# Kernel tuning notes

Measured on AMD Instinct MI355X. Metric: run time of the kernel, lower is better.

Reference implementation:

```python
import jax, jax.numpy as jnp
import numpy as np


def setup_inputs() -> dict:
    key = jax.random.key(0)
    ks = jax.random.split(key, 8)
    B, N, F, H, D, C = 16, 8192, 512, 512, 256, 2
    s = 0.02
    return {
        "h": jax.random.normal(ks[0], (B, N, F), dtype=jnp.float32),
        "W1": jax.random.normal(ks[1], (F, H), dtype=jnp.float32) * s,
        "b1": jnp.zeros((H,), jnp.float32),
        "Wa": jax.random.normal(ks[2], (H, D), dtype=jnp.float32) * s,
        "ba": jnp.zeros((D,), jnp.float32),
        "Wb": jax.random.normal(ks[3], (H, D), dtype=jnp.float32) * s,
        "bb": jnp.zeros((D,), jnp.float32),
        "Wc": jax.random.normal(ks[4], (D, 1), dtype=jnp.float32) * s,
        "bc": jnp.zeros((1,), jnp.float32),
        "Wcls": jax.random.normal(ks[5], (H, C), dtype=jnp.float32) * s,
        "bcls": jnp.zeros((C,), jnp.float32),
    }


def reference(h, W1, b1, Wa, ba, Wb, bb, Wc, bc, Wcls, bcls):
    # h: [B, N, F]  (B bags, N instances each)
    h1 = jax.nn.relu(jnp.einsum("bnf,fh->bnh", h, W1) + b1)        # [B,N,H]
    a = jnp.tanh(jnp.einsum("bnh,hd->bnd", h1, Wa) + ba)           # [B,N,D]
    g = jax.nn.sigmoid(jnp.einsum("bnh,hd->bnd", h1, Wb) + bb)     # [B,N,D]
    A = jnp.einsum("bnd,dk->bnk", a * g, Wc) + bc                  # [B,N,1]
    A_raw = jnp.swapaxes(A, 1, 2)                                  # [B,1,N]
    A_sm = jax.nn.softmax(A_raw, axis=-1)                          # [B,1,N]
    M = jnp.einsum("bkn,bnh->bkh", A_sm, h1)                       # [B,1,H]
    context = jnp.mean(M, axis=0)                                  # [1,H]  (sum / len(h_list))
    logits = context @ Wcls + bcls                                 # [1,C]
    Y_prob = jax.nn.softmax(logits, axis=1)
    Y_hat = jnp.argmax(logits, axis=1, keepdims=True)
    return (logits, Y_prob, Y_hat, A_raw, M)
```

## Files before the change

### kernel.cpp

```cpp
#include <hip/hip_runtime.h>
#include <math.h>

typedef short bf16x8 __attribute__((ext_vector_type(8)));
typedef float f32x4  __attribute__((ext_vector_type(4)));

#define GLOAD_LDS16(SRC, DST) \
  __builtin_amdgcn_global_load_lds((const __attribute__((address_space(1))) void*)(SRC), \
      (__attribute__((address_space(3))) void*)(DST), 16, 0, 0)

#define WAITVM(N) asm volatile("s_waitcnt vmcnt(" #N ")" ::: "memory")
#define WAITLGKM0 asm volatile("s_waitcnt lgkmcnt(0)" ::: "memory")
#define BARRIER() do { __builtin_amdgcn_s_barrier(); asm volatile("" ::: "memory"); } while (0)

__device__ __forceinline__ unsigned short f2bf(float f) {
  union { float f; unsigned u; } v; v.f = f;
  unsigned r = v.u + 0x7FFFu + ((v.u >> 16) & 1u);
  return (unsigned short)(r >> 16);
}
__device__ __forceinline__ float bf2f(unsigned short s) {
  union { unsigned u; float f; } v; v.u = ((unsigned)s) << 16;
  return v.f;
}
__device__ __forceinline__ unsigned pk2bf(float lo, float hi) {
  unsigned r;
  asm("v_cvt_pk_bf16_f32 %0, %1, %2" : "=v"(r) : "v"(lo), "v"(hi));
  return r;
}
__device__ __forceinline__ float fexp2(float x) {
  float r; asm("v_exp_f32 %0, %1" : "=v"(r) : "v"(x)); return r;
}
__device__ __forceinline__ float frcp(float x) {
  float r; asm("v_rcp_f32 %0, %1" : "=v"(r) : "v"(x)); return r;
}
#define LOG2E 1.44269504f
__device__ __forceinline__ float fexp(float x) { return fexp2(x * LOG2E); }


__global__ void carp_wpack(const float* __restrict__ W1, const float* __restrict__ Wa,
                           const float* __restrict__ Wb,
                           unsigned short* __restrict__ W1T_pk, unsigned short* __restrict__ WabT_pk) {
  int t = blockIdx.x * 256 + threadIdx.x;
  int mat = t >> 15;
  int gid = t & 32767;
  int g = gid & 511;
  int kt = (gid >> 9) & 15;
  int p = gid >> 13;
  int s = g >> 6, l = g & 63;
  int j = p * 128 + s * 16 + (l & 15);
  int k = kt * 32 + (l >> 4) * 8;
  unsigned short v[8];
  if (mat == 0) {
#pragma unroll
    for (int e = 0; e < 8; ++e) v[e] = f2bf(W1[(size_t)(k + e) * 512 + j]);
    *(uint4*)(W1T_pk + (size_t)gid * 8) = *(const uint4*)v;
  } else {
    int d = j >> 1;
    const float* Wx = (j & 1) ? Wb : Wa;
#pragma unroll
    for (int e = 0; e < 8; ++e) v[e] = f2bf(Wx[(size_t)(k + e) * 256 + d]);
    *(uint4*)(WabT_pk + (size_t)gid * 8) = *(const uint4*)v;
  }
}

__launch_bounds__(512, 2)
__global__ void carp_gemm1(const float* __restrict__ h, const unsigned short* __restrict__ W1T_pk,
                           const float* __restrict__ b1, unsigned short* __restrict__ h1_pk) {
  __shared__ __align__(16) unsigned short lds[49152];
  int bid0 = blockIdx.x;
  int bid = (bid0 & 7) * 256 + (bid0 >> 3);
  int bn = bid & 3, bm = bid >> 2;
  int brow = bm * 256;
  int tid = threadIdx.x, lane = tid & 63, wid = tid >> 6;
  int wr = wid >> 1, wc = wid & 1;

  f32x4 acc[4][4] = {};
  float4 ar[8];

  int r0 = tid >> 4;
  int chunk = tid & 15;
  const float* hbase = h + (size_t)(brow + r0) * 512 + chunk * 4;
  int kgA = (chunk & 7) >> 1, r16A = r0 & 15;
  int aw_const = (chunk >> 3) * 8192 + (r0 >> 4) * 1024 + kgA * 256
               + ((r16A * 16) ^ (kgA << 5)) + (chunk & 1) * 8;
  int aread_lane = (lane >> 4) * 256 + (((lane & 15) * 16) ^ ((lane >> 4) << 5));

#define G1_LOADA(TP) do { \
  _Pragma("unroll") for (int q = 0; q < 8; ++q) \
    ar[q] = *(const float4*)(hbase + (size_t)(q * 32) * 512 + (TP) * 64); \
  } while (0)
#define G1_WRITEA(TP) do { \
  char* dstA = (char*)lds + ((TP) & 1) * 32768; \
  _Pragma("unroll") for (int q = 0; q < 8; ++q) { \
    uint2 wv; wv.x = pk2bf(ar[q].x, ar[q].y); wv.y = pk2bf(ar[q].z, ar[q].w); \
    *(uint2*)(dstA + (q >> 2) * 16384 + (q & 3) * 2048 + aw_const) = wv; \
  } } while (0)
#define G1_STAGEB(TP, BUF) do { \
  _Pragma("unroll") for (int t2 = 0; t2 < 2; ++t2) \
    GLOAD_LDS16(W1T_pk + ((size_t)(bn * 16 + (TP) * 2 + t2) * 512 + wid * 64 + lane) * 8, \
                (char*)lds + 65536 + (BUF) * 16384 + t2 * 8192 + (size_t)wid * 1024); \
  } while (0)

  G1_LOADA(0);
  WAITVM(0);
  G1_WRITEA(0);
  G1_STAGEB(0, 0);
  G1_LOADA(1);
  WAITLGKM0;

#pragma unroll 1
  for (int tp = 0; tp < 8; ++tp) {
    if (tp < 7) G1_STAGEB(tp + 1, (tp + 1) & 1);
    if (tp < 7) { WAITVM(10); } else { WAITVM(0); }
    BARRIER();
    const char* Abase = (const char*)lds + (tp & 1) * 32768;
    const char* Bbase = (const char*)lds + 65536 + (tp & 1) * 16384;
#pragma unroll
    for (int tt = 0; tt < 2; ++tt) {
      bf16x8 afr[4], bfr[4];
#pragma unroll
      for (int m = 0; m < 4; ++m) {
        int gs = wr * 4 + m;
        afr[m] = *(const bf16x8*)(Abase + (gs >> 3) * 16384 + tt * 8192
                                  + (gs & 7) * 1024 + aread_lane);
      }
#pragma unroll
      for (int n = 0; n < 4; ++n)
        bfr[n] = *(const bf16x8*)(Bbase + tt * 8192 + (size_t)((wc * 4 + n) * 64 + lane) * 16);
#pragma unroll
      for (int m = 0; m < 4; ++m)
#pragma unroll
        for (int n = 0; n < 4; ++n)
          acc[m][n] = __builtin_amdgcn_mfma_f32_16x16x32_bf16(afr[m], bfr[n], acc[m][n], 0, 0, 0);
    }
    if (tp < 7) { WAITVM(2); G1_WRITEA(tp + 1); }
    if (tp < 6) G1_LOADA(tp + 2);
    WAITLGKM0;
    BARRIER();
  }
#undef G1_LOADA
#undef G1_WRITEA
#undef G1_STAGEB

  unsigned short* img = lds;
#pragma unroll
  for (int n = 0; n < 4; ++n) {
    int cl = wc * 64 + n * 16 + (lane & 15);
    float bias = b1[bn * 128 + cl];
    int ktc = cl >> 5, c32 = cl & 31;
#pragma unroll
    for (int m = 0; m < 4; ++m)
#pragma unroll
      for (int j = 0; j < 4; ++j) {
        int r = wr * 64 + m * 16 + (lane >> 4) * 4 + j;
        float v = acc[m][n][j] + bias;
        v = v > 0.f ? v : 0.f;
        int gidx = (r >> 7) * 2048 + ktc * 512 + ((r & 127) >> 4) * 64 + (c32 >> 3) * 16 + (r & 15);
        img[(size_t)gidx * 8 + (c32 & 7)] = f2bf(v);
      }
  }
  __syncthreads();
#pragma unroll
  for (int i = 0; i < 8; ++i) {
    int g = i * 512 + tid;
    int P = (2 * bm + (g >> 11)) * 16 + bn * 4 + ((g >> 9) & 3);
    *(uint4*)(h1_pk + ((size_t)P * 512 + (g & 511)) * 8) = *(const uint4*)(img + (size_t)g * 8);
  }
}

#define G2_STAGE(T32, HALF, BUF) do { \
  _Pragma("unroll") for (int q = 0; q < 2; ++q) { \
    int c = wid * 2 + q; \
    int P = (2 * bm + (c >> 3)) * 16 + (T32); \
    GLOAD_LDS16(h1_pk + ((size_t)P * 512 + (c & 7) * 64 + lane) * 8, \
                (char*)lds + (BUF) * 32768 + (HALF) * 16384 + (size_t)c * 1024); \
  } \
  GLOAD_LDS16(WabT_pk + ((size_t)(bn * 16 + (T32)) * 512 + wid * 64 + lane) * 8, \
              (char*)lds + 65536 + (BUF) * 16384 + (HALF) * 8192 + (size_t)wid * 1024); \
  } while (0)

__launch_bounds__(512, 2)
__global__ void carp_gemm2(const unsigned short* __restrict__ h1_pk, const unsigned short* __restrict__ WabT_pk,
                           const float* __restrict__ ba, const float* __restrict__ bb,
                           const float* __restrict__ Wc, float* __restrict__ A_part) {
  __shared__ __align__(16) unsigned short lds[49152];
  int bid0 = blockIdx.x;
  int bid = (bid0 & 7) * 256 + (bid0 >> 3);
  int bn = bid & 3, bm = bid >> 2;
  int tid = threadIdx.x, lane = tid & 63, wid = tid >> 6;
  int wr = wid >> 1, wc = wid & 1;
  f32x4 acc[4][4] = {};

  G2_STAGE(0, 0, 0); G2_STAGE(1, 1, 0);
#pragma unroll 1
  for (int kt = 0; kt < 8; ++kt) {
    int cur = kt & 1, nxt = cur ^ 1;
    if (kt < 7) { G2_STAGE(2 * kt + 2, 0, nxt); G2_STAGE(2 * kt + 3, 1, nxt); }
    if (kt < 7) { WAITVM(6); } else { WAITVM(0); }
    BARRIER();
#pragma unroll
    for (int tt = 0; tt < 2; ++tt) {
      const char* Ab = (const char*)lds + cur * 32768 + tt * 16384;
      const char* Bb = (const char*)lds + 65536 + cur * 16384 + tt * 8192;
      bf16x8 afr[4], bfr[4];
#pragma unroll
      for (int m = 0; m < 4; ++m)
        afr[m] = *(const bf16x8*)(Ab + (size_t)((wr * 4 + m) * 64 + lane) * 16);
#pragma unroll
      for (int n = 0; n < 4; ++n)
        bfr[n] = *(const bf16x8*)(Bb + (size_t)((wc * 4 + n) * 64 + lane) * 16);
#pragma unroll
      for (int m = 0; m < 4; ++m)
#pragma unroll
        for (int n = 0; n < 4; ++n)
          acc[m][n] = __builtin_amdgcn_mfma_f32_16x16x32_bf16(afr[m], bfr[n], acc[m][n], 0, 0, 0);
    }
    WAITLGKM0;
    BARRIER();
  }

  int brow = bm * 256, bcol = bn * 128;
  int odd = lane & 1;
  float kA = odd ? -LOG2E : -2.f * LOG2E;
  float c1 = odd ? 1.f : 2.f;
  float c0 = odd ? 0.f : -1.f;
  float rowpart[4][4] = {};
#pragma unroll
  for (int n = 0; n < 4; ++n) {
    int cg = bcol + wc * 64 + n * 16 + (lane & 15);
    int d = cg >> 1;
    float bias = (cg & 1) ? bb[d] : ba[d];
    float wcd = Wc[d];
#pragma unroll
    for (int m = 0; m < 4; ++m)
#pragma unroll
      for (int j = 0; j < 4; ++j) {
        float v = acc[m][n][j] + bias;
        float av = c1 * frcp(1.f + fexp2(kA * v)) + c0;
        float pv = av * __shfl_xor(av, 1, 64);
        rowpart[m][j] += pv * wcd;
      }
  }
#pragma unroll
  for (int m = 0; m < 4; ++m)
#pragma unroll
    for (int j = 0; j < 4; ++j) {
      float t = rowpart[m][j];
      t += __shfl_xor(t, 2, 64);
      t += __shfl_xor(t, 4, 64);
      t += __shfl_xor(t, 8, 64);
      rowpart[m][j] = t;
    }
  if ((lane & 15) == 0) {
    int slot = bn * 2 + wc;
#pragma unroll
    for (int m = 0; m < 4; ++m)
#pragma unroll
      for (int j = 0; j < 4; ++j) {
        int row = brow + wr * 64 + m * 16 + (lane >> 4) * 4 + j;
        A_part[(size_t)row * 8 + slot] = rowpart[m][j];
      }
  }
}
#undef G2_STAGE

__global__ void carp_softmax(const float* __restrict__ A_part, const float* __restrict__ bc,
                             float* __restrict__ A_raw_out, float* __restrict__ A_sm) {
  __shared__ float sv[8192];
  __shared__ float red[256];
  int b = blockIdx.x, tid = threadIdx.x;
  float bcv = bc[0];
  float lmax = -1e30f;
  for (int i = tid; i < 8192; i += 256) {
    const float4* p = (const float4*)(A_part + (size_t)(b * 8192 + i) * 8);
    float4 x = p[0], y = p[1];
    float s = ((x.x + x.y) + (x.z + x.w)) + ((y.x + y.y) + (y.z + y.w)) + bcv;
    sv[i] = s;
    A_raw_out[b * 8192 + i] = s;
    lmax = fmaxf(lmax, s);
  }
  red[tid] = lmax;
  for (int s = 128; s > 0; s >>= 1) { __syncthreads(); if (tid < s) red[tid] = fmaxf(red[tid], red[tid + s]); }
  __syncthreads();
  float mx = red[0];
  __syncthreads();
  float lsum = 0.f;
  for (int i = tid; i < 8192; i += 256) {
    float e = fexp(sv[i] - mx);
    sv[i] = e;
    lsum += e;
  }
  red[tid] = lsum;
  for (int s = 128; s > 0; s >>= 1) { __syncthreads(); if (tid < s) red[tid] += red[tid + s]; }
  __syncthreads();
  float inv = 1.f / red[0];
  for (int i = tid; i < 8192; i += 256) A_sm[b * 8192 + i] = sv[i] * inv;
}

__global__ void carp_mkernel(const unsigned short* __restrict__ h1_pk, const float* __restrict__ A_sm,
                             float* __restrict__ Mpart) {
  __shared__ float sw[128];
  int bm = blockIdx.x;
  int tid = threadIdx.x;
  if (tid < 128) sw[tid] = A_sm[bm * 128 + tid];
  __syncthreads();
  int l = tid & 63;
  float acc[4][8] = {};
#pragma unroll
  for (int tq = 0; tq < 4; ++tq) {
    int tt = (tid >> 6) * 4 + tq;
#pragma unroll
    for (int s = 0; s < 8; ++s) {
      const unsigned short* gp = h1_pk + ((size_t)(bm * 16 + tt) * 512 + s * 64 + l) * 8;
      uint4 raw = *(const uint4*)gp;
      const unsigned short* pv = (const unsigned short*)&raw;
      float w = sw[s * 16 + (l & 15)];
#pragma unroll
      for (int e = 0; e < 8; ++e) acc[tq][e] += w * bf2f(pv[e]);
    }
  }
#pragma unroll
  for (int tq = 0; tq < 4; ++tq)
#pragma unroll
    for (int e = 0; e < 8; ++e) {
      float t = acc[tq][e];
      t += __shfl_xor(t, 1, 64);
      t += __shfl_xor(t, 2, 64);
      t += __shfl_xor(t, 4, 64);
      t += __shfl_xor(t, 8, 64);
      acc[tq][e] = t;
    }
  if ((l & 15) == 0) {
    int cc = (l >> 4) & 3;
#pragma unroll
    for (int tq = 0; tq < 4; ++tq) {
      int tt = (tid >> 6) * 4 + tq;
      float* mp = Mpart + (size_t)bm * 512 + tt * 32 + cc * 8;
#pragma unroll
      for (int e = 0; e < 8; ++e) mp[e] = acc[tq][e];
    }
  }
}

__global__ void carp_final(const float* __restrict__ Mpart, const float* __restrict__ Wcls,
                           const float* __restrict__ bcls, float* __restrict__ out) {
  __shared__ float ctx[512];
  int t = threadIdx.x;
  float c = 0.f;
  for (int b = 0; b < 16; ++b) {
    float s = 0.f;
    for (int p = 0; p < 64; ++p) s += Mpart[((size_t)(b * 64 + p) << 9) + t];
    out[131077 + b * 512 + t] = s;
    c += s;
  }
  ctx[t] = c * (1.f / 16.f);
  __syncthreads();
  if (t < 64) {
    float p0 = 0.f, p1 = 0.f;
    for (int hh = t; hh < 512; hh += 64) {
      float cv = ctx[hh];
      p0 += cv * Wcls[hh * 2];
      p1 += cv * Wcls[hh * 2 + 1];
    }
    for (int m = 1; m < 64; m <<= 1) { p0 += __shfl_xor(p0, m, 64); p1 += __shfl_xor(p1, m, 64); }
    if (t == 0) {
      float l0 = p0 + bcls[0], l1 = p1 + bcls[1];
      out[0] = l0; out[1] = l1;
      float mx = fmaxf(l0, l1);
      float e0 = expf(l0 - mx), e1 = expf(l1 - mx);
      float s = e0 + e1;
      out[2] = e0 / s; out[3] = e1 / s;
      out[4] = (l1 > l0) ? 1.0f : 0.0f;
    }
  }
}

extern "C" void kernel_launch(void* const* d_in, const int* in_sizes, int n_in,
                              void* d_out, int out_size, void* d_ws, size_t ws_size,
                              hipStream_t stream) {
  const float* h    = (const float*)d_in[0];
  const float* W1   = (const float*)d_in[1];
  const float* b1   = (const float*)d_in[2];
  const float* Wa   = (const float*)d_in[3];
  const float* ba   = (const float*)d_in[4];
  const float* Wb   = (const float*)d_in[5];
  const float* bb   = (const float*)d_in[6];
  const float* Wc   = (const float*)d_in[7];
  const float* bc   = (const float*)d_in[8];
  const float* Wcls = (const float*)d_in[9];
  const float* bcls = (const float*)d_in[10];
  float* out = (float*)d_out;

  char* ws = (char*)d_ws;
  unsigned short* h1_pk   = (unsigned short*)(ws);
  unsigned short* W1T_pk  = (unsigned short*)(ws + 134217728);
  unsigned short* WabT_pk = (unsigned short*)(ws + 134742016);
  float* A_part           = (float*)(ws + 135266304);
  float* A_sm             = (float*)(ws + 139460608);
  float* Mpart            = (float*)(ws + 135266304);

  carp_wpack  <<<256,  256, 0, stream>>>(W1, Wa, Wb, W1T_pk, WabT_pk);
  carp_gemm1  <<<2048, 512, 0, stream>>>(h, W1T_pk, b1, h1_pk);
  carp_gemm2  <<<2048, 512, 0, stream>>>(h1_pk, WabT_pk, ba, bb, Wc, A_part);
  carp_softmax<<<16,   256, 0, stream>>>(A_part, bc, out + 5, A_sm);
  carp_mkernel<<<1024, 256, 0, stream>>>(h1_pk, A_sm, Mpart);
  carp_final  <<<1,    512, 0, stream>>>(Mpart, Wcls, bcls, out);
}
```

Before: 364.7 us.

## Widen GEMM tiles to 256x256 and add LDS swizzle for A tile

```diff
diff --git a/kernel.cpp b/kernel.cpp
--- a/kernel.cpp
+++ b/kernel.cpp
@@ -65,15 +65,15 @@
 __launch_bounds__(512, 2)
 __global__ void carp_gemm1(const float* __restrict__ h, const unsigned short* __restrict__ W1T_pk,
                            const float* __restrict__ b1, unsigned short* __restrict__ h1_pk) {
-  __shared__ __align__(16) unsigned short lds[49152];
+  __shared__ __align__(16) unsigned short lds[65536];
   int bid0 = blockIdx.x;
-  int bid = (bid0 & 7) * 256 + (bid0 >> 3);
-  int bn = bid & 3, bm = bid >> 2;
+  int bid = (bid0 & 7) * 128 + (bid0 >> 3);
+  int bn = bid & 1, bm = bid >> 1;
   int brow = bm * 256;
   int tid = threadIdx.x, lane = tid & 63, wid = tid >> 6;
   int wr = wid >> 1, wc = wid & 1;
 
-  f32x4 acc[4][4] = {};
+  f32x4 acc[4][8] = {};
   float4 ar[8];
 
   int r0 = tid >> 4;
@@ -81,7 +81,7 @@
   const float* hbase = h + (size_t)(brow + r0) * 512 + chunk * 4;
   int kgA = (chunk & 7) >> 1, r16A = r0 & 15;
   int aw_const = (chunk >> 3) * 8192 + (r0 >> 4) * 1024 + kgA * 256
-               + ((r16A * 16) ^ (kgA << 5)) + (chunk & 1) * 8;
+               + ((r16A * 16) ^ (kgA << 5) ^ ((chunk >> 3) << 4)) + (chunk & 1) * 8;
   int aread_lane = (lane >> 4) * 256 + (((lane & 15) * 16) ^ ((lane >> 4) << 5));
 
 #define G1_LOADA(TP) do { \
@@ -95,10 +95,12 @@
     *(uint2*)(dstA + (q >> 2) * 16384 + (q & 3) * 2048 + aw_const) = wv; \
   } } while (0)
 #define G1_STAGEB(TP, BUF) do { \
-  _Pragma("unroll") for (int t2 = 0; t2 < 2; ++t2) \
-    GLOAD_LDS16(W1T_pk + ((size_t)(bn * 16 + (TP) * 2 + t2) * 512 + wid * 64 + lane) * 8, \
-                (char*)lds + 65536 + (BUF) * 16384 + t2 * 8192 + (size_t)wid * 1024); \
-  } while (0)
+  _Pragma("unroll") for (int q = 0; q < 4; ++q) { \
+    int c = wid * 4 + q; \
+    int pn = 2 * bn + ((c & 15) >> 3); \
+    GLOAD_LDS16(W1T_pk + ((size_t)(pn * 16 + (TP) * 2 + (c >> 4)) * 512 + (c & 7) * 64 + lane) * 8, \
+                (char*)lds + 65536 + (BUF) * 32768 + (size_t)c * 1024); \
+  } } while (0)
 
   G1_LOADA(0);
   WAITVM(0);
@@ -110,29 +112,30 @@
 #pragma unroll 1
   for (int tp = 0; tp < 8; ++tp) {
     if (tp < 7) G1_STAGEB(tp + 1, (tp + 1) & 1);
-    if (tp < 7) { WAITVM(10); } else { WAITVM(0); }
+    if (tp < 7) { WAITVM(12); } else { WAITVM(0); }
     BARRIER();
     const char* Abase = (const char*)lds + (tp & 1) * 32768;
-    const char* Bbase = (const char*)lds + 65536 + (tp & 1) * 16384;
+    const char* Bbase = (const char*)lds + 65536 + (tp & 1) * 32768;
 #pragma unroll
     for (int tt = 0; tt < 2; ++tt) {
-      bf16x8 afr[4], bfr[4];
+      bf16x8 afr[4], bfr[8];
 #pragma unroll
       for (int m = 0; m < 4; ++m) {
         int gs = wr * 4 + m;
         afr[m] = *(const bf16x8*)(Abase + (gs >> 3) * 16384 + tt * 8192
-                                  + (gs & 7) * 1024 + aread_lane);
+                                  + (gs & 7) * 1024 + (aread_lane ^ (tt << 4)));
       }
 #pragma unroll
-      for (int n = 0; n < 4; ++n)
-        bfr[n] = *(const bf16x8*)(Bbase + tt * 8192 + (size_t)((wc * 4 + n) * 64 + lane) * 16);
+      for (int n = 0; n < 8; ++n)
+        bfr[n] = *(const bf16x8*)(Bbase + tt * 16384 + wc * 8192
+                                  + (size_t)(n * 64 + lane) * 16);
 #pragma unroll
       for (int m = 0; m < 4; ++m)
 #pragma unroll
-        for (int n = 0; n < 4; ++n)
+        for (int n = 0; n < 8; ++n)
           acc[m][n] = __builtin_amdgcn_mfma_f32_16x16x32_bf16(afr[m], bfr[n], acc[m][n], 0, 0, 0);
     }
-    if (tp < 7) { WAITVM(2); G1_WRITEA(tp + 1); }
+    if (tp < 7) { WAITVM(4); G1_WRITEA(tp + 1); }
     if (tp < 6) G1_LOADA(tp + 2);
     WAITLGKM0;
     BARRIER();
@@ -143,9 +146,9 @@
 
   unsigned short* img = lds;
 #pragma unroll
-  for (int n = 0; n < 4; ++n) {
-    int cl = wc * 64 + n * 16 + (lane & 15);
-    float bias = b1[bn * 128 + cl];
+  for (int n = 0; n < 8; ++n) {
+    int cl = wc * 128 + n * 16 + (lane & 15);
+    float bias = b1[bn * 256 + cl];
     int ktc = cl >> 5, c32 = cl & 31;
 #pragma unroll
     for (int m = 0; m < 4; ++m)
@@ -154,15 +157,15 @@
         int r = wr * 64 + m * 16 + (lane >> 4) * 4 + j;
         float v = acc[m][n][j] + bias;
         v = v > 0.f ? v : 0.f;
-        int gidx = (r >> 7) * 2048 + ktc * 512 + ((r & 127) >> 4) * 64 + (c32 >> 3) * 16 + (r & 15);
+        int gidx = (r >> 7) * 4096 + ktc * 512 + ((r & 127) >> 4) * 64 + (c32 >> 3) * 16 + (r & 15);
         img[(size_t)gidx * 8 + (c32 & 7)] = f2bf(v);
       }
   }
   __syncthreads();
 #pragma unroll
-  for (int i = 0; i < 8; ++i) {
+  for (int i = 0; i < 16; ++i) {
     int g = i * 512 + tid;
-    int P = (2 * bm + (g >> 11)) * 16 + bn * 4 + ((g >> 9) & 3);
+    int P = (2 * bm + (g >> 12)) * 16 + bn * 8 + ((g >> 9) & 7);
     *(uint4*)(h1_pk + ((size_t)P * 512 + (g & 511)) * 8) = *(const uint4*)(img + (size_t)g * 8);
   }
 }
@@ -174,59 +177,64 @@
     GLOAD_LDS16(h1_pk + ((size_t)P * 512 + (c & 7) * 64 + lane) * 8, \
                 (char*)lds + (BUF) * 32768 + (HALF) * 16384 + (size_t)c * 1024); \
   } \
-  GLOAD_LDS16(WabT_pk + ((size_t)(bn * 16 + (T32)) * 512 + wid * 64 + lane) * 8, \
-              (char*)lds + 65536 + (BUF) * 16384 + (HALF) * 8192 + (size_t)wid * 1024); \
-  } while (0)
+  _Pragma("unroll") for (int q = 0; q < 2; ++q) { \
+    int c2 = wid * 2 + q; \
+    int pn = 2 * bn + (c2 >> 3); \
+    GLOAD_LDS16(WabT_pk + ((size_t)(pn * 16 + (T32)) * 512 + (c2 & 7) * 64 + lane) * 8, \
+                (char*)lds + 65536 + (BUF) * 32768 + (HALF) * 16384 + (size_t)c2 * 1024); \
+  } } while (0)
 
 __launch_bounds__(512, 2)
 __global__ void carp_gemm2(const unsigned short* __restrict__ h1_pk, const unsigned short* __restrict__ WabT_pk,
                            const float* __restrict__ ba, const float* __restrict__ bb,
                            const float* __restrict__ Wc, float* __restrict__ A_part) {
-  __shared__ __align__(16) unsigned short lds[49152];
+  __shared__ __align__(16) unsigned short lds[65536];
   int bid0 = blockIdx.x;
-  int bid = (bid0 & 7) * 256 + (bid0 >> 3);
-  int bn = bid & 3, bm = bid >> 2;
+  int bid = (bid0 & 7) * 128 + (bid0 >> 3);
+  int bn = bid & 1, bm = bid >> 1;
   int tid = threadIdx.x, lane = tid & 63, wid = tid >> 6;
   int wr = wid >> 1, wc = wid & 1;
-  f32x4 acc[4][4] = {};
+
+  f32x4 acc[4][8] = {};
 
   G2_STAGE(0, 0, 0); G2_STAGE(1, 1, 0);
+
 #pragma unroll 1
   for (int kt = 0; kt < 8; ++kt) {
     int cur = kt & 1, nxt = cur ^ 1;
     if (kt < 7) { G2_STAGE(2 * kt + 2, 0, nxt); G2_STAGE(2 * kt + 3, 1, nxt); }
-    if (kt < 7) { WAITVM(6); } else { WAITVM(0); }
+    if (kt < 7) { WAITVM(8); } else { WAITVM(0); }
     BARRIER();
 #pragma unroll
     for (int tt = 0; tt < 2; ++tt) {
       const char* Ab = (const char*)lds + cur * 32768 + tt * 16384;
-      const char* Bb = (const char*)lds + 65536 + cur * 16384 + tt * 8192;
-      bf16x8 afr[4], bfr[4];
+      const char* Bb = (const char*)lds + 65536 + cur * 32768 + tt * 16384 + wc * 8192;
+      bf16x8 afr[4], bfr[8];
 #pragma unroll
       for (int m = 0; m < 4; ++m)
         afr[m] = *(const bf16x8*)(Ab + (size_t)((wr * 4 + m) * 64 + lane) * 16);
 #pragma unroll
-      for (int n = 0; n < 4; ++n)
-        bfr[n] = *(const bf16x8*)(Bb + (size_t)((wc * 4 + n) * 64 + lane) * 16);
+      for (int n = 0; n < 8; ++n)
+        bfr[n] = *(const bf16x8*)(Bb + (size_t)(n * 64 + lane) * 16);
 #pragma unroll
       for (int m = 0; m < 4; ++m)
 #pragma unroll
-        for (int n = 0; n < 4; ++n)
+        for (int n = 0; n < 8; ++n)
           acc[m][n] = __builtin_amdgcn_mfma_f32_16x16x32_bf16(afr[m], bfr[n], acc[m][n], 0, 0, 0);
     }
     WAITLGKM0;
     BARRIER();
   }
 
-  int brow = bm * 256, bcol = bn * 128;
+  int brow = bm * 256, bcol = bn * 256;
   int odd = lane & 1;
   float kA = odd ? -LOG2E : -2.f * LOG2E;
   float c1 = odd ? 1.f : 2.f;
   float c0 = odd ? 0.f : -1.f;
   float rowpart[4][4] = {};
 #pragma unroll
-  for (int n = 0; n < 4; ++n) {
-    int cg = bcol + wc * 64 + n * 16 + (lane & 15);
+  for (int n = 0; n < 8; ++n) {
+    int cg = bcol + wc * 128 + n * 16 + (lane & 15);
     int d = cg >> 1;
     float bias = (cg & 1) ? bb[d] : ba[d];
     float wcd = Wc[d];
@@ -257,7 +265,7 @@
 #pragma unroll
       for (int j = 0; j < 4; ++j) {
         int row = brow + wr * 64 + m * 16 + (lane >> 4) * 4 + j;
-        A_part[(size_t)row * 8 + slot] = rowpart[m][j];
+        A_part[(size_t)row * 4 + slot] = rowpart[m][j];
       }
   }
 }
@@ -271,9 +279,8 @@
   float bcv = bc[0];
   float lmax = -1e30f;
   for (int i = tid; i < 8192; i += 256) {
-    const float4* p = (const float4*)(A_part + (size_t)(b * 8192 + i) * 8);
-    float4 x = p[0], y = p[1];
-    float s = ((x.x + x.y) + (x.z + x.w)) + ((y.x + y.y) + (y.z + y.w)) + bcv;
+    float4 x = *(const float4*)(A_part + (size_t)(b * 8192 + i) * 4);
+    float s = (x.x + x.y) + (x.z + x.w) + bcv;
     sv[i] = s;
     A_raw_out[b * 8192 + i] = s;
     lmax = fmaxf(lmax, s);
@@ -399,8 +406,8 @@
   float* Mpart            = (float*)(ws + 135266304);
 
   carp_wpack  <<<256,  256, 0, stream>>>(W1, Wa, Wb, W1T_pk, WabT_pk);
-  carp_gemm1  <<<2048, 512, 0, stream>>>(h, W1T_pk, b1, h1_pk);
-  carp_gemm2  <<<2048, 512, 0, stream>>>(h1_pk, WabT_pk, ba, bb, Wc, A_part);
+  carp_gemm1  <<<1024, 512, 0, stream>>>(h, W1T_pk, b1, h1_pk);
+  carp_gemm2  <<<1024, 512, 0, stream>>>(h1_pk, WabT_pk, ba, bb, Wc, A_part);
   carp_softmax<<<16,   256, 0, stream>>>(A_part, bc, out + 5, A_sm);
   carp_mkernel<<<1024, 256, 0, stream>>>(h1_pk, A_sm, Mpart);
   carp_final  <<<1,    512, 0, stream>>>(Mpart, Wcls, bcls, out);
```

New measurement: 310.9 us. -14.7%, faster.
